# Optimization experiments

Measured on AMD Instinct MI355X. Metric: run time of the kernel, lower is better.

The kernel has to match this reference:

```python
import jax, jax.numpy as jnp
import numpy as np

WINDOW = 2  # window_size

def _causal_window_conv(x, W, b):
    # x: [B,T,D_in], W: [WINDOW, D_in, D_out], b: [D_out]
    # equivalent to left-padding x by WINDOW-1 zeros and a 'valid' conv
    B, T, _ = x.shape
    xp = jnp.pad(x, ((0, 0), (WINDOW - 1, 0), (0, 0)))  # [B, T+WINDOW-1, D_in]
    out = b
    for k in range(WINDOW):
        out = out + jnp.einsum('btd,de->bte', xp[:, k:k + T], W[k])
    return out  # [B,T,D_out]

def setup_inputs() -> dict:
    key = jax.random.key(0)
    ks = jax.random.split(key, 4)
    B, T, Din, Dout = 8, 4096, 256, 256
    scale = 0.05
    x = jax.random.normal(ks[0], (B, T, Din), dtype=jnp.float32)
    W_z = jax.random.normal(ks[1], (WINDOW, Din, Dout), dtype=jnp.float32) * scale
    W_f = jax.random.normal(ks[2], (WINDOW, Din, Dout), dtype=jnp.float32) * scale
    W_o = jax.random.normal(ks[3], (WINDOW, Din, Dout), dtype=jnp.float32) * scale
    b_z = jnp.zeros((Dout,), dtype=jnp.float32)
    b_f = jnp.zeros((Dout,), dtype=jnp.float32)
    b_o = jnp.zeros((Dout,), dtype=jnp.float32)
    return {"x": x, "W_z": W_z, "W_f": W_f, "W_o": W_o,
            "b_z": b_z, "b_f": b_f, "b_o": b_o}

def reference(x, W_z, W_f, W_o, b_z, b_f, b_o):
    # QRNN with fo-pooling (Bradbury et al. 2016), return_sequences=True
    z = jnp.tanh(_causal_window_conv(x, W_z, b_z))          # [B,T,D]
    f = jax.nn.sigmoid(_causal_window_conv(x, W_f, b_f))    # [B,T,D]
    o = jax.nn.sigmoid(_causal_window_conv(x, W_o, b_o))    # [B,T,D]

    def step(c, zfo):
        z_t, f_t, o_t = zfo
        c = f_t * c + (1.0 - f_t) * z_t   # fo-pooling recurrence
        h = o_t * c
        return c, h

    c0 = jnp.zeros(z.shape[::2], dtype=z.dtype)  # [B,D]
    # time-major for scan
    zfo = (z.transpose(1, 0, 2), f.transpose(1, 0, 2), o.transpose(1, 0, 2))
    _, hs = jax.lax.scan(step, c0, zfo)
    return hs.transpose(1, 0, 2)  # [B,T,D]
```

## Files before the change

kernel.cpp:

```cpp
#include <hip/hip_runtime.h>
#include <hip/hip_bf16.h>
#include <hip/hip_fp16.h>

#define BDIM 8
#define TDIM 4096
#define DDIM 256
#define MDIM (BDIM * TDIM)
#define NCHUNK 256
#define LCHUNK (TDIM / NCHUNK)

typedef _Float16 f16x8 __attribute__((ext_vector_type(8)));
typedef _Float16 f16x4 __attribute__((ext_vector_type(4)));
typedef float f32x4 __attribute__((ext_vector_type(4)));

__device__ __forceinline__ float sigmoid_(float x) {
    return 1.0f / (1.0f + __expf(-x));
}
__device__ __forceinline__ float tanh_(float x) {
    return 2.0f / (1.0f + __expf(-2.0f * x)) - 1.0f;
}

#define GLOAD_LDS16(g, l)                                                    \
    __builtin_amdgcn_global_load_lds(                                        \
        (const __attribute__((address_space(1))) void*)(g),                  \
        (__attribute__((address_space(3))) void*)(l), 16, 0, 0)

__global__ __launch_bounds__(64) void convert_x(const float* __restrict__ x,
                                                _Float16* __restrict__ xpad) {
    const int tp = blockIdx.x;
    const int b = blockIdx.y;
    const int q = threadIdx.x;
    float4 v = make_float4(0.f, 0.f, 0.f, 0.f);
    if (tp > 0)
        v = *(const float4*)(x + ((size_t)b * TDIM + tp - 1) * DDIM + q * 4);
    f16x4 h;
    h[0] = (_Float16)v.x; h[1] = (_Float16)v.y;
    h[2] = (_Float16)v.z; h[3] = (_Float16)v.w;
    *(f16x4*)(xpad + ((size_t)b * (TDIM + 1) + tp) * DDIM + q * 4) = h;
}

__global__ __launch_bounds__(256) void convert_w(
    const float* __restrict__ Wz, const float* __restrict__ Wf,
    const float* __restrict__ Wo, _Float16* __restrict__ Wt) {
    const int idx = blockIdx.x * 256 + threadIdx.x;
    const int n = idx & 255;
    const int kin = (idx >> 8) & 255;
    const int w = (idx >> 16) & 1;
    const int g = idx >> 17;
    const float* W = (g == 0) ? Wz : (g == 1) ? Wf : Wo;
    const float v = W[(size_t)w * 65536 + (size_t)kin * 256 + n];
    Wt[((size_t)g * 256 + n) * 512 + w * 256 + kin] = (_Float16)v;
}

__global__ __launch_bounds__(256) void gates_mfma(
    const _Float16* __restrict__ xpad, const _Float16* __restrict__ Wt,
    const float* __restrict__ bz, const float* __restrict__ bfv,
    const float* __restrict__ bo,
    _Float16* __restrict__ zbuf, _Float16* __restrict__ fbuf,
    _Float16* __restrict__ obuf) {
    const int gate = blockIdx.z;
    const int m0 = blockIdx.x * 128;
    const int n0 = blockIdx.y * 128;
    const int tid = threadIdx.x;
    const int lane = tid & 63;
    const int wave = tid >> 6;
    const int wr = wave >> 1;
    const int wc = wave & 1;

    __shared__ __align__(16) char smem[40960];

    const int s = wave * 64 + lane;
    const int r1 = s >> 2;
    const int kc = (s & 3) * 8;

    const int b = m0 >> 12;
    const int t0 = m0 & (TDIM - 1);

    const _Float16* srcA1 =
        xpad + ((size_t)b * (TDIM + 1) + t0 + r1) * DDIM + kc;
    const _Float16* srcA2 = srcA1 + (size_t)64 * DDIM;
    const _Float16* srcB1 = Wt + ((size_t)gate * 256 + n0 + r1) * 512 + kc;
    const _Float16* srcB2 = srcB1 + (size_t)64 * 512;

    f32x4 acc[4][4] = {};
    const int am = lane & 15;
    const int kq = (lane >> 4) * 8;

    {
        char* dA = smem + wave * 1024;
        char* dB = smem + 8192 + wave * 1024;
        GLOAD_LDS16(srcA1, dA);
        GLOAD_LDS16(srcA2, dA + 4096);
        GLOAD_LDS16(srcB1, dB);
        GLOAD_LDS16(srcB2, dB + 4096);
    }

    for (int it = 0; it < 16; ++it) {
        __syncthreads();
        const int cur = it & 1;
        if (it < 15) {
            const int k1 = (it + 1) * 32;
            char* dA = smem + (cur ^ 1) * 16384 + wave * 1024;
            char* dB = smem + (cur ^ 1) * 16384 + 8192 + wave * 1024;
            GLOAD_LDS16(srcA1 + k1, dA);
            GLOAD_LDS16(srcA2 + k1, dA + 4096);
            GLOAD_LDS16(srcB1 + k1, dB);
            GLOAD_LDS16(srcB2 + k1, dB + 4096);
        }
        const _Float16* Ab = (const _Float16*)(smem + cur * 16384);
        const _Float16* Bb = (const _Float16*)(smem + cur * 16384 + 8192);

        f16x8 a[4], bb[4];
#pragma unroll
        for (int i = 0; i < 4; ++i)
            a[i] = *(const f16x8*)(Ab + (wr * 64 + i * 16 + am) * 32 + kq);
#pragma unroll
        for (int j = 0; j < 4; ++j)
            bb[j] = *(const f16x8*)(Bb + (wc * 64 + j * 16 + am) * 32 + kq);
#pragma unroll
        for (int i = 0; i < 4; ++i)
#pragma unroll
            for (int j = 0; j < 4; ++j)
                acc[i][j] = __builtin_amdgcn_mfma_f32_16x16x32_f16(
                    a[i], bb[j], acc[i][j], 0, 0, 0);
    }

    __syncthreads();

    const float* bias = (gate == 0) ? bz : (gate == 1) ? bfv : bo;
    _Float16* outp = (gate == 0) ? zbuf : (gate == 1) ? fbuf : obuf;
    _Float16* eb = (_Float16*)smem + wave * 5120;
    const int rq = (lane >> 4) * 4;
#pragma unroll
    for (int j = 0; j < 4; ++j) {
        const int gc = n0 + wc * 64 + j * 16 + am;
        const float bj = bias[gc];
#pragma unroll
        for (int i = 0; i < 4; ++i) {
            f32x4 v = acc[i][j];
#pragma unroll
            for (int r = 0; r < 4; ++r) {
                const float val = v[r] + bj;
                const float act = (gate == 0) ? tanh_(val) : sigmoid_(val);
                eb[(i * 16 + rq + r) * 80 + j * 16 + am] = (_Float16)act;
            }
        }
    }
    __syncthreads();

    const int rrow = lane >> 3;
    const int rcol = (lane & 7) * 8;
#pragma unroll
    for (int rr = 0; rr < 8; ++rr) {
        const int row = rr * 8 + rrow;
        f16x8 v = *(const f16x8*)(eb + row * 80 + rcol);
        const size_t gm = (size_t)(m0 + wr * 64 + row);
        *(f16x8*)(outp + gm * DDIM + n0 + wc * 64 + rcol) = v;
    }
}

__global__ __launch_bounds__(256) void scan_pass1(
    const _Float16* __restrict__ zbuf, const _Float16* __restrict__ fbuf,
    float* __restrict__ aggA, float* __restrict__ aggB) {
    const int idx = blockIdx.x * 256 + threadIdx.x;
    const int d8 = idx & 31;
    const int chunk = (idx >> 5) & (NCHUNK - 1);
    const int b = idx >> 13;

    const size_t row0 = (size_t)b * TDIM + (size_t)chunk * LCHUNK;
    const int4* zp = (const int4*)zbuf + row0 * 32 + d8;
    const int4* fp = (const int4*)fbuf + row0 * 32 + d8;

    float A[8], c[8];
#pragma unroll
    for (int e = 0; e < 8; ++e) { A[e] = 1.0f; c[e] = 0.0f; }

    for (int i = 0; i < LCHUNK; ++i) {
        int4 fv = *fp;
        int4 zv = *zp;
        const _Float16* fh = (const _Float16*)&fv;
        const _Float16* zh = (const _Float16*)&zv;
#pragma unroll
        for (int e = 0; e < 8; ++e) {
            const float f = (float)fh[e];
            const float z = (float)zh[e];
            A[e] *= f;
            c[e] = f * c[e] + (1.0f - f) * z;
        }
        fp += 32;
        zp += 32;
    }
    ((float4*)aggA)[(size_t)idx * 2 + 0] = make_float4(A[0], A[1], A[2], A[3]);
    ((float4*)aggA)[(size_t)idx * 2 + 1] = make_float4(A[4], A[5], A[6], A[7]);
    ((float4*)aggB)[(size_t)idx * 2 + 0] = make_float4(c[0], c[1], c[2], c[3]);
    ((float4*)aggB)[(size_t)idx * 2 + 1] = make_float4(c[4], c[5], c[6], c[7]);
}

__global__ __launch_bounds__(256) void carry_scan(
    const float* __restrict__ aggA, const float* __restrict__ aggB,
    float* __restrict__ carry) {
    const int g = blockIdx.x * 256 + threadIdx.x;
    const int d = g & 255;
    const int b = g >> 8;
    const size_t base = (size_t)b * NCHUNK * 256 + d;

    float c = 0.0f;
    for (int ch0 = 0; ch0 < NCHUNK; ch0 += 8) {
        float A[8], Bv[8];
#pragma unroll
        for (int u = 0; u < 8; ++u) {
            const size_t p = base + (size_t)(ch0 + u) * 256;
            A[u] = aggA[p];
            Bv[u] = aggB[p];
        }
#pragma unroll
        for (int u = 0; u < 8; ++u) {
            const size_t p = base + (size_t)(ch0 + u) * 256;
            carry[p] = c;
            c = A[u] * c + Bv[u];
        }
    }
}

__global__ __launch_bounds__(256) void scan_pass2(
    const _Float16* __restrict__ zbuf, const _Float16* __restrict__ fbuf,
    const _Float16* __restrict__ obuf, const float* __restrict__ carry,
    float* __restrict__ out) {
    const int idx = blockIdx.x * 256 + threadIdx.x;
    const int d8 = idx & 31;
    const int chunk = (idx >> 5) & (NCHUNK - 1);
    const int b = idx >> 13;

    float c[8];
    float4 c0 = ((const float4*)carry)[(size_t)idx * 2];
    float4 c1 = ((const float4*)carry)[(size_t)idx * 2 + 1];
    c[0] = c0.x; c[1] = c0.y; c[2] = c0.z; c[3] = c0.w;
    c[4] = c1.x; c[5] = c1.y; c[6] = c1.z; c[7] = c1.w;

    const size_t row0 = (size_t)b * TDIM + (size_t)chunk * LCHUNK;
    const int4* zp = (const int4*)zbuf + row0 * 32 + d8;
    const int4* fp = (const int4*)fbuf + row0 * 32 + d8;
    const int4* op = (const int4*)obuf + row0 * 32 + d8;
    float4* hp = (float4*)out + row0 * 64 + d8 * 2;

    for (int i = 0; i < LCHUNK; ++i) {
        int4 fv = *fp;
        int4 zv = *zp;
        int4 ov = *op;
        const _Float16* fh = (const _Float16*)&fv;
        const _Float16* zh = (const _Float16*)&zv;
        const _Float16* oh = (const _Float16*)&ov;
        float h[8];
#pragma unroll
        for (int e = 0; e < 8; ++e) {
            const float f = (float)fh[e];
            const float z = (float)zh[e];
            c[e] = f * c[e] + (1.0f - f) * z;
            h[e] = (float)oh[e] * c[e];
        }
        hp[0] = make_float4(h[0], h[1], h[2], h[3]);
        hp[1] = make_float4(h[4], h[5], h[6], h[7]);
        fp += 32;
        zp += 32;
        op += 32;
        hp += 64;
    }
}

extern "C" void kernel_launch(void* const* d_in, const int* in_sizes, int n_in,
                              void* d_out, int out_size, void* d_ws,
                              size_t ws_size, hipStream_t stream) {
    const float* x = (const float*)d_in[0];
    const float* Wz = (const float*)d_in[1];
    const float* Wf = (const float*)d_in[2];
    const float* Wo = (const float*)d_in[3];
    const float* bz = (const float*)d_in[4];
    const float* bfv = (const float*)d_in[5];
    const float* bo = (const float*)d_in[6];
    float* out = (float*)d_out;

    char* p = (char*)d_ws;
    _Float16* xpad = (_Float16*)p;  p += (size_t)BDIM * (TDIM + 1) * DDIM * 2;
    _Float16* Wt = (_Float16*)p;    p += (size_t)3 * 256 * 512 * 2;
    _Float16* zbuf = (_Float16*)p;  p += (size_t)MDIM * DDIM * 2;
    _Float16* fbuf = (_Float16*)p;  p += (size_t)MDIM * DDIM * 2;
    _Float16* obuf = (_Float16*)p;  p += (size_t)MDIM * DDIM * 2;
    float* aggA = (float*)p;        p += (size_t)BDIM * NCHUNK * DDIM * 4;
    float* aggB = (float*)p;        p += (size_t)BDIM * NCHUNK * DDIM * 4;
    float* carry = (float*)p;

    convert_x<<<dim3(TDIM + 1, BDIM), 64, 0, stream>>>(x, xpad);
    convert_w<<<(3 * 2 * 256 * 256) / 256, 256, 0, stream>>>(Wz, Wf, Wo, Wt);

    gates_mfma<<<dim3(MDIM / 128, DDIM / 128, 3), 256, 0, stream>>>(
        xpad, Wt, bz, bfv, bo, zbuf, fbuf, obuf);

    scan_pass1<<<(BDIM * NCHUNK * 32) / 256, 256, 0, stream>>>(zbuf, fbuf,
                                                               aggA, aggB);
    carry_scan<<<(BDIM * DDIM) / 256, 256, 0, stream>>>(aggA, aggB, carry);
    scan_pass2<<<(BDIM * NCHUNK * 32) / 256, 256, 0, stream>>>(zbuf, fbuf,
                                                               obuf, carry, out);
}
```

Measured before the change: 176.3 us.

## Triple-buffer gate GEMM with swizzled LDS layout and explicit waitcnt scheduling

The gates MFMA GEMM moves from double to triple buffering of LDS tiles, with two stages prefetched up front. Each iteration now waits on explicit vmcnt and barrier instructions rather than a full __syncthreads. K-chunks in LDS are XOR-swizzled to reduce bank conflicts on the f16x8 fragment reads. The epilogue row pitch changes from 80 to 72 halves, and MFMA blocks get raised wave priority. In exchange it uses more LDS, which can lower occupancy, and relies on hand-counted waitcnts being correct.

New measurement: 173.4 us. About the same (-1.7%).

```diff
diff --git a/kernel.cpp b/kernel.cpp
--- a/kernel.cpp
+++ b/kernel.cpp
@@ -67,11 +67,11 @@
     const int wr = wave >> 1;
     const int wc = wave & 1;
 
-    __shared__ __align__(16) char smem[40960];
+    __shared__ __align__(16) char smem[49152];
 
     const int s = wave * 64 + lane;
     const int r1 = s >> 2;
-    const int kc = (s & 3) * 8;
+    const int kc = (((s & 3) ^ ((s >> 3) & 3))) * 8;
 
     const int b = m0 >> 12;
     const int t0 = m0 & (TDIM - 1);
@@ -82,54 +82,64 @@
     const _Float16* srcB1 = Wt + ((size_t)gate * 256 + n0 + r1) * 512 + kc;
     const _Float16* srcB2 = srcB1 + (size_t)64 * 512;
 
+#define STAGE_(slot, t)                                                      \
+    {                                                                        \
+        char* dA = smem + (slot) * 16384 + wave * 1024;                      \
+        char* dB = smem + (slot) * 16384 + 8192 + wave * 1024;               \
+        GLOAD_LDS16(srcA1 + (t) * 32, dA);                                   \
+        GLOAD_LDS16(srcA2 + (t) * 32, dA + 4096);                            \
+        GLOAD_LDS16(srcB1 + (t) * 32, dB);                                   \
+        GLOAD_LDS16(srcB2 + (t) * 32, dB + 4096);                            \
+    }
+
     f32x4 acc[4][4] = {};
     const int am = lane & 15;
-    const int kq = (lane >> 4) * 8;
-
-    {
-        char* dA = smem + wave * 1024;
-        char* dB = smem + 8192 + wave * 1024;
-        GLOAD_LDS16(srcA1, dA);
-        GLOAD_LDS16(srcA2, dA + 4096);
-        GLOAD_LDS16(srcB1, dB);
-        GLOAD_LDS16(srcB2, dB + 4096);
-    }
-
+    const int kswz = (((lane >> 4) ^ ((lane >> 1) & 3))) * 8;
+
+    STAGE_(0, 0);
+    STAGE_(1, 1);
+
+#pragma unroll
     for (int it = 0; it < 16; ++it) {
-        __syncthreads();
-        const int cur = it & 1;
-        if (it < 15) {
-            const int k1 = (it + 1) * 32;
-            char* dA = smem + (cur ^ 1) * 16384 + wave * 1024;
-            char* dB = smem + (cur ^ 1) * 16384 + 8192 + wave * 1024;
-            GLOAD_LDS16(srcA1 + k1, dA);
-            GLOAD_LDS16(srcA2 + k1, dA + 4096);
-            GLOAD_LDS16(srcB1 + k1, dB);
-            GLOAD_LDS16(srcB2 + k1, dB + 4096);
-        }
-        const _Float16* Ab = (const _Float16*)(smem + cur * 16384);
-        const _Float16* Bb = (const _Float16*)(smem + cur * 16384 + 8192);
+        if (it < 15)
+            asm volatile("s_waitcnt vmcnt(4)" ::: "memory");
+        else
+            asm volatile("s_waitcnt vmcnt(0)" ::: "memory");
+        __builtin_amdgcn_s_barrier();
+        __builtin_amdgcn_sched_barrier(0);
+        if (it < 14) STAGE_((it + 2) % 3, it + 2);
+        __builtin_amdgcn_sched_barrier(0);
+
+        const _Float16* Ab = (const _Float16*)(smem + (it % 3) * 16384);
+        const _Float16* Bb = (const _Float16*)(smem + (it % 3) * 16384 + 8192);
 
         f16x8 a[4], bb[4];
 #pragma unroll
         for (int i = 0; i < 4; ++i)
-            a[i] = *(const f16x8*)(Ab + (wr * 64 + i * 16 + am) * 32 + kq);
+            a[i] = *(const f16x8*)(Ab + (wr * 64 + i * 16 + am) * 32 + kswz);
 #pragma unroll
         for (int j = 0; j < 4; ++j)
-            bb[j] = *(const f16x8*)(Bb + (wc * 64 + j * 16 + am) * 32 + kq);
+            bb[j] = *(const f16x8*)(Bb + (wc * 64 + j * 16 + am) * 32 + kswz);
+
+        asm volatile("s_waitcnt lgkmcnt(0)" ::: "memory");
+        __builtin_amdgcn_sched_barrier(0);
+        __builtin_amdgcn_s_setprio(1);
 #pragma unroll
         for (int i = 0; i < 4; ++i)
 #pragma unroll
             for (int j = 0; j < 4; ++j)
                 acc[i][j] = __builtin_amdgcn_mfma_f32_16x16x32_f16(
                     a[i], bb[j], acc[i][j], 0, 0, 0);
-    }
+        __builtin_amdgcn_s_setprio(0);
+        __builtin_amdgcn_sched_barrier(0);
+    }
+#undef STAGE_
 
     __syncthreads();
 
     const float* bias = (gate == 0) ? bz : (gate == 1) ? bfv : bo;
     _Float16* outp = (gate == 0) ? zbuf : (gate == 1) ? fbuf : obuf;
-    _Float16* eb = (_Float16*)smem + wave * 5120;
+    _Float16* eb = (_Float16*)smem + wave * 4608;
     const int rq = (lane >> 4) * 4;
 #pragma unroll
     for (int j = 0; j < 4; ++j) {
@@ -142,7 +152,7 @@
             for (int r = 0; r < 4; ++r) {
                 const float val = v[r] + bj;
                 const float act = (gate == 0) ? tanh_(val) : sigmoid_(val);
-                eb[(i * 16 + rq + r) * 80 + j * 16 + am] = (_Float16)act;
+                eb[(i * 16 + rq + r) * 72 + j * 16 + am] = (_Float16)act;
             }
         }
     }
@@ -153,7 +163,7 @@
 #pragma unroll
     for (int rr = 0; rr < 8; ++rr) {
         const int row = rr * 8 + rrow;
-        f16x8 v = *(const f16x8*)(eb + row * 80 + rcol);
+        f16x8 v = *(const f16x8*)(eb + row * 72 + rcol);
         const size_t gm = (size_t)(m0 + wr * 64 + row);
         *(f16x8*)(outp + gm * DDIM + n0 + wc * 64 + rcol) = v;
     }
```
